# Kernel tuning notes

Measured on AMD Instinct MI355X. Metric: run time of the kernel, lower is better.

The kernel has to match this reference:

```python
import jax, jax.numpy as jnp
import numpy as np

N_NODES = 50000
N_EDGES = 600000
D = 128  # input_nf = output_nf = hidden_nf
EDGE_IN = 2 * D + 1   # source, target, radial
NODE_IN = 2 * D       # x, agg


def _glorot(key, shape):
    fan_in, fan_out = shape[0], shape[1]
    lim = float(np.sqrt(6.0 / (fan_in + fan_out)))
    return jax.random.uniform(key, shape, jnp.float32, -lim, lim)


def setup_inputs() -> dict:
    key = jax.random.key(0)
    ks = jax.random.split(key, 16)
    h = jax.random.normal(ks[0], (N_NODES, D), jnp.float32)
    edge_index = jax.random.randint(ks[1], (2, N_EDGES), 0, N_NODES, jnp.int64 if jax.config.read('jax_enable_x64') else jnp.int32)
    coord = jax.random.uniform(ks[2], (N_NODES, 3), jnp.float32)
    l = jnp.array([10.0, 10.0, 10.0], jnp.float32)  # periodic box lengths (non-trainable buffer)
    return {
        'h': h, 'edge_index': edge_index, 'coord': coord, 'num_nodes': N_NODES, 'l': l,
        # edge_mlp: Linear(257,128) SiLU Linear(128,128) SiLU
        'We1': _glorot(ks[3], (EDGE_IN, D)), 'be1': jnp.zeros((D,), jnp.float32),
        'We2': _glorot(ks[4], (D, D)),       'be2': jnp.zeros((D,), jnp.float32),
        # node_mlp: Linear(256,128) SiLU Linear(128,128)
        'Wn1': _glorot(ks[5], (NODE_IN, D)), 'bn1': jnp.zeros((D,), jnp.float32),
        'Wn2': _glorot(ks[6], (D, D)),       'bn2': jnp.zeros((D,), jnp.float32),
        # coord_mlp: Linear(128,128) SiLU Linear(128,1, bias=False, xavier gain=0.001)
        'Wc1': _glorot(ks[7], (D, D)),       'bc1': jnp.zeros((D,), jnp.float32),
        'Wc2': _glorot(ks[8], (D, 1)) * 0.001,
    }


def reference(h, edge_index, coord, num_nodes, l,
              We1, be1, We2, be2, Wn1, bn1, Wn2, bn2, Wc1, bc1, Wc2):
    row, col = edge_index[0], edge_index[1]

    # coord2radial with periodic minimum-image wrap
    diff = coord[row] - coord[col]                       # [E, 3]
    diff = jnp.where(diff > 0.5 * l, diff - l, diff)
    diff = jnp.where(diff < -0.5 * l, diff + l, diff)
    radial = jnp.sum(diff * diff, axis=1, keepdims=True)  # [E, 1]

    # edge model: gather -> concat -> 2-layer SiLU MLP
    eh = jnp.concatenate([h[row], h[col], radial], axis=1)  # [E, 257]
    eh = jax.nn.silu(eh @ We1 + be1)
    edge_feat = jax.nn.silu(eh @ We2 + be2)                 # [E, 128]

    # coord model: trans/agg computed in the original but discarded (dead code);
    # only the periodic remainder of coord is returned.
    coord_out = jnp.remainder(coord, l)

    # node model: scatter-add edge features into nodes, then MLP + residual
    agg = jax.ops.segment_sum(edge_feat, row, num_segments=num_nodes)  # [N, 128]
    nh = jnp.concatenate([h, agg], axis=1)                              # [N, 256]
    nh = jax.nn.silu(nh @ Wn1 + bn1)
    h_out = h + (nh @ Wn2 + bn2)

    return h_out, coord_out, edge_feat
```

## Files before the change

kernel.cpp:

```cpp
#include <hip/hip_runtime.h>
#include <math.h>

#define D 128
#define SXS 264
#define SHS 132
#define SFS 132

typedef unsigned int u32;
typedef unsigned short u16;
typedef __attribute__((ext_vector_type(8))) short bf16x8;
typedef __attribute__((ext_vector_type(4))) float f32x4;

__device__ __forceinline__ float bfl(u32 u) { return __uint_as_float(u << 16); }
__device__ __forceinline__ float bfh(u32 u) { return __uint_as_float(u & 0xFFFF0000u); }
__device__ __forceinline__ u16 f2bf(float f) {
    u32 u = __float_as_uint(f);
    return (u16)((u + 0x7FFFu + ((u >> 16) & 1u)) >> 16);
}
__device__ __forceinline__ u32 cvt_pk_bf16(float lo, float hi) {
    u32 r;
    asm("v_cvt_pk_bf16_f32 %0, %1, %2" : "=v"(r) : "v"(lo), "v"(hi));
    return r;
}
__device__ __forceinline__ u16 cvt1_bf16(float v) { return (u16)cvt_pk_bf16(v, v); }
__device__ __forceinline__ float silu_f(float x) { return x / (1.0f + __expf(-x)); }

__global__ void coord_kernel(const float* __restrict__ coord,
                             const float* __restrict__ lbox,
                             float* __restrict__ out, int n3) {
    int i = blockIdx.x * 256 + threadIdx.x;
    if (i < n3) {
        float ld = lbox[i % 3];
        float c = coord[i];
        float r = fmodf(c, ld);
        if (r < 0.f) r += ld;
        out[i] = r;
    }
}

__global__ void prep_weights(const float* __restrict__ We1, const float* __restrict__ We2,
                             const float* __restrict__ Wn1, const float* __restrict__ Wn2,
                             u16* __restrict__ wt) {
    int i = blockIdx.x * 256 + threadIdx.x;
    if (i < 32768)        { int n = i >> 8, k = i & 255;              wt[i] = f2bf(We1[(size_t)k*D + n]); }
    else if (i < 49152)   { int j = i - 32768; int n = j >> 7, k = j & 127; wt[i] = f2bf(We2[(size_t)k*D + n]); }
    else if (i < 81920)   { int j = i - 49152; int n = j >> 8, k = j & 255; wt[i] = f2bf(Wn1[(size_t)k*D + n]); }
    else if (i < 98304)   { int j = i - 81920; int n = j >> 7, k = j & 127; wt[i] = f2bf(Wn2[(size_t)k*D + n]); }
}

__global__ void hist_kernel(const int* __restrict__ ei, int* __restrict__ cnt, int E) {
    int e = blockIdx.x * 256 + threadIdx.x;
    if (e < E) atomicAdd(&cnt[ei[e]], 1);
}

__global__ void scan1_kernel(const int* __restrict__ cnt, int* __restrict__ offs,
                             int* __restrict__ bsum, int n ) {
    __shared__ int s[256];
    int t = threadIdx.x, b = blockIdx.x;
    int base = b * 1024 + t * 4;
    int v[4];
    #pragma unroll
    for (int i = 0; i < 4; ++i) { int idx = base + i; v[i] = (idx < n - 1) ? cnt[idx] : 0; }
    int lsum = v[0] + v[1] + v[2] + v[3];
    s[t] = lsum; __syncthreads();
    #pragma unroll
    for (int off = 1; off < 256; off <<= 1) {
        int x = (t >= off) ? s[t - off] : 0; __syncthreads();
        s[t] += x; __syncthreads();
    }
    int run = s[t] - lsum;
    #pragma unroll
    for (int i = 0; i < 4; ++i) { int idx = base + i; if (idx < n) offs[idx] = run; run += v[i]; }
    if (t == 255) bsum[b] = s[255];
}

__global__ void scan2_kernel(int* __restrict__ bsum, int nb) {
    __shared__ int s[64];
    int t = threadIdx.x;
    int orig = (t < nb) ? bsum[t] : 0;
    s[t] = orig; __syncthreads();
    #pragma unroll
    for (int off = 1; off < 64; off <<= 1) {
        int x = (t >= off) ? s[t - off] : 0; __syncthreads();
        s[t] += x; __syncthreads();
    }
    if (t < nb) bsum[t] = s[t] - orig;
}

__global__ void scan3_kernel(int* __restrict__ offs, const int* __restrict__ bsum,
                             int* __restrict__ cursor, int n) {
    int i = blockIdx.x * 256 + threadIdx.x;
    if (i < n) {
        int v = offs[i] + bsum[i >> 10];
        offs[i] = v;
        if (i < n - 1) cursor[i] = v;
    }
}

__global__ void scatter_kernel(const int* __restrict__ ei, int* __restrict__ cursor,
                               int* __restrict__ perm, int4* __restrict__ edata, int E) {
    int e = blockIdx.x * 256 + threadIdx.x;
    if (e < E) {
        int r = ei[e];
        int c = ei[(size_t)E + e];
        int p = atomicAdd(&cursor[r], 1);
        if (edata) edata[p] = make_int4(e, r, c, 0);
        else perm[p] = e;
    }
}

__global__ __launch_bounds__(256, 4) void pq_kernel(
    const float* __restrict__ h, const u16* __restrict__ wt,
    const float* __restrict__ be1,
    u16* __restrict__ Pt, u16* __restrict__ Qt,
    int* __restrict__ cursor, int N)
{
    __shared__ __align__(16) u16 sA[64 * SHS];
    __shared__ __align__(16) u16 sO[64 * SHS];

    const int t = threadIdx.x;
    const int lane = t & 63;
    const int wid = t >> 6;
    const int n0 = blockIdx.x * 64;

    if (t < 64) { int zi = n0 + t; if (zi < N) cursor[zi] = 0; }

    {
        const int e = t & 63, q = t >> 6;
        int ng = n0 + e; int ns = (ng < N) ? ng : N - 1;
        const float4* src = (const float4*)(h + (size_t)ns * D + q * 32);
        u16* dst = sA + e * SHS + q * 32;
        #pragma unroll
        for (int c = 0; c < 4; ++c) {
            float4 a = src[2 * c], b = src[2 * c + 1];
            *(uint4*)(dst + c * 8) = make_uint4(cvt_pk_bf16(a.x, a.y), cvt_pk_bf16(a.z, a.w),
                                               cvt_pk_bf16(b.x, b.y), cvt_pk_bf16(b.z, b.w));
        }
    }
    __syncthreads();

    const int lrow = lane & 15;
    const int kg = lane >> 4;
    const int g4 = kg * 4;
    const int nbase = wid * 32;

    f32x4 accP[4][2] = {}, accQ[4][2] = {};
    {
        bf16x8 Bt[8], Bm[8];
        #pragma unroll
        for (int nn = 0; nn < 2; ++nn)
            #pragma unroll
            for (int s = 0; s < 4; ++s) {
                const u16* bp = wt + (size_t)(nbase + nn * 16 + lrow) * 256 + s * 32 + kg * 8;
                Bt[nn * 4 + s] = *(const bf16x8*)bp;
                Bm[nn * 4 + s] = *(const bf16x8*)(bp + 128);
            }
        #pragma unroll
        for (int s = 0; s < 4; ++s) {
            bf16x8 a[4];
            #pragma unroll
            for (int m = 0; m < 4; ++m)
                a[m] = *(const bf16x8*)(sA + (m * 16 + lrow) * SHS + s * 32 + kg * 8);
            #pragma unroll
            for (int m = 0; m < 4; ++m)
                #pragma unroll
                for (int nn = 0; nn < 2; ++nn) {
                    accP[m][nn] = __builtin_amdgcn_mfma_f32_16x16x32_bf16(a[m], Bt[nn * 4 + s], accP[m][nn], 0, 0, 0);
                    accQ[m][nn] = __builtin_amdgcn_mfma_f32_16x16x32_bf16(a[m], Bm[nn * 4 + s], accQ[m][nn], 0, 0, 0);
                }
        }
    }

    #pragma unroll
    for (int nn = 0; nn < 2; ++nn) {
        int outc = nbase + nn * 16 + lrow;
        float bb = be1[outc];
        #pragma unroll
        for (int m = 0; m < 4; ++m)
            #pragma unroll
            for (int r = 0; r < 4; ++r)
                sO[(m * 16 + g4 + r) * SHS + outc] = cvt1_bf16(accP[m][nn][r] + bb);
    }
    __syncthreads();
    {
        const int f4 = t & 15, rb = t >> 4;
        #pragma unroll
        for (int p = 0; p < 4; ++p) {
            int row = rb + p * 16;
            int ng = n0 + row;
            if (ng < N)
                *(uint4*)(Pt + (size_t)ng * D + f4 * 8) = *(const uint4*)(sO + row * SHS + f4 * 8);
        }
    }
    __syncthreads();
    #pragma unroll
    for (int nn = 0; nn < 2; ++nn) {
        int outc = nbase + nn * 16 + lrow;
        #pragma unroll
        for (int m = 0; m < 4; ++m)
            #pragma unroll
            for (int r = 0; r < 4; ++r)
                sO[(m * 16 + g4 + r) * SHS + outc] = cvt1_bf16(accQ[m][nn][r]);
    }
    __syncthreads();
    {
        const int f4 = t & 15, rb = t >> 4;
        #pragma unroll
        for (int p = 0; p < 4; ++p) {
            int row = rb + p * 16;
            int ng = n0 + row;
            if (ng < N)
                *(uint4*)(Qt + (size_t)ng * D + f4 * 8) = *(const uint4*)(sO + row * SHS + f4 * 8);
        }
    }
}

__global__ __launch_bounds__(256, 8) void edge_pq_kernel(
    const u16* __restrict__ Pt, const u16* __restrict__ Qt,
    const int* __restrict__ ei, const int* __restrict__ perm,
    const int4* __restrict__ edata,
    const float* __restrict__ coord, const float* __restrict__ lbox,
    const u16* __restrict__ wt, const float* __restrict__ We1,
    const float* __restrict__ be2,
    float* __restrict__ ef_out, float* __restrict__ aggf, int E)
{
    __shared__ __align__(16) u16 uni[64 * SHS];
    __shared__ int srow[64], scol[64], sEid[64];
    __shared__ float sRad[64];
    __shared__ float sW[128];
    u16* sH1 = uni;
    u16* sE16 = uni;

    const int t = threadIdx.x;
    const int lane = t & 63;
    const int wid = t >> 6;

    int p0;
    {
        const int nwg = gridDim.x;
        const int orig = blockIdx.x;
        const int q = nwg >> 3, r = nwg & 7;
        const int xcd = orig & 7, idx = orig >> 3;
        const int tile = (xcd < r ? xcd * (q + 1) : r * (q + 1) + (xcd - r) * q) + idx;
        p0 = tile * 64;
    }

    if (t < 64) {
        int slot = p0 + t;
        bool valid = slot < E;
        int cs = valid ? slot : (E - 1);
        int eg, rr, cc;
        if (edata) {
            int4 ed = edata[cs];
            eg = ed.x; rr = ed.y; cc = ed.z;
        } else {
            eg = perm[cs];
            rr = ei[eg];
            cc = ei[(size_t)E + eg];
        }
        sEid[t] = valid ? eg : -1;
        srow[t] = rr;
        scol[t] = cc;
        float rad = 0.f;
        #pragma unroll
        for (int d3 = 0; d3 < 3; ++d3) {
            float df = coord[(size_t)rr * 3 + d3] - coord[(size_t)cc * 3 + d3];
            float ld = lbox[d3];
            df = (df >  0.5f * ld) ? df - ld : df;
            df = (df < -0.5f * ld) ? df + ld : df;
            rad += df * df;
        }
        sRad[t] = rad;
    } else if (t < 192) {
        sW[t - 64] = We1[(size_t)256 * D + (t - 64)];
    }
    __syncthreads();

    {
        const int e = t & 63, q = t >> 6;
        const u16* Pp = Pt + (size_t)srow[e] * D;
        const u16* Qp = Qt + (size_t)scol[e] * D;
        const float rad = sRad[e];
        #pragma unroll
        for (int c0 = 0; c0 < 4; ++c0) {
            int j0 = q * 32 + c0 * 8;
            uint4 pu = *(const uint4*)(Pp + j0);
            uint4 qu = *(const uint4*)(Qp + j0);
            u32 pa[4] = {pu.x, pu.y, pu.z, pu.w};
            u32 qa[4] = {qu.x, qu.y, qu.z, qu.w};
            u32 ow[4];
            #pragma unroll
            for (int k = 0; k < 4; ++k) {
                float w0 = sW[j0 + 2 * k], w1 = sW[j0 + 2 * k + 1];
                float v0 = silu_f(bfl(pa[k]) + bfl(qa[k]) + rad * w0);
                float v1 = silu_f(bfh(pa[k]) + bfh(qa[k]) + rad * w1);
                ow[k] = cvt_pk_bf16(v0, v1);
            }
            *(uint4*)(sH1 + e * SHS + j0) = make_uint4(ow[0], ow[1], ow[2], ow[3]);
        }
    }
    __syncthreads();

    const int lrow = lane & 15;
    const int kg = lane >> 4;
    const int g4 = kg * 4;
    const int nbase = wid * 32;

    f32x4 acc2[4][2] = {};
    {
        bf16x8 B2[8];
        #pragma unroll
        for (int nn = 0; nn < 2; ++nn)
            #pragma unroll
            for (int s = 0; s < 4; ++s)
                B2[nn * 4 + s] = *(const bf16x8*)(wt + 32768 + (size_t)(nbase + nn * 16 + lrow) * 128 + s * 32 + kg * 8);
        #pragma unroll
        for (int s = 0; s < 4; ++s) {
            bf16x8 a[4];
            #pragma unroll
            for (int m = 0; m < 4; ++m)
                a[m] = *(const bf16x8*)(sH1 + (m * 16 + lrow) * SHS + s * 32 + kg * 8);
            #pragma unroll
            for (int m = 0; m < 4; ++m)
                #pragma unroll
                for (int nn = 0; nn < 2; ++nn)
                    acc2[m][nn] = __builtin_amdgcn_mfma_f32_16x16x32_bf16(a[m], B2[nn * 4 + s], acc2[m][nn], 0, 0, 0);
        }
    }
    __syncthreads();

    #pragma unroll
    for (int nn = 0; nn < 2; ++nn) {
        int outc = nbase + nn * 16 + lrow;
        float bb = be2[outc];
        #pragma unroll
        for (int m = 0; m < 4; ++m)
            #pragma unroll
            for (int r = 0; r < 4; ++r)
                sE16[(m * 16 + g4 + r) * SHS + outc] = cvt1_bf16(silu_f(acc2[m][nn][r] + bb));
    }
    __syncthreads();

    {
        const int ct = t & 127;
        const int half = t >> 7;
        const int ebeg = half * 32, eend = ebeg + 32;
        float run = 0.f;
        int prev = srow[ebeg];
        for (int e = ebeg; e < eend; ++e) {
            int r = srow[e];
            if (r != prev) {
                if (run != 0.f) atomicAdd(&aggf[(size_t)prev * D + ct], run);
                run = 0.f; prev = r;
            }
            int eg = sEid[e];
            if (eg >= 0) {
                float v = __uint_as_float((u32)sE16[e * SHS + ct] << 16);
                __builtin_nontemporal_store(v, &ef_out[(size_t)eg * D + ct]);
                run += v;
            }
        }
        if (run != 0.f) atomicAdd(&aggf[(size_t)prev * D + ct], run);
    }
}

__global__ __launch_bounds__(256, 3) void edge_fb_kernel(
    const float* __restrict__ h,
    const int* __restrict__ ei, const int* __restrict__ perm,
    const float* __restrict__ coord, const float* __restrict__ lbox,
    const u16* __restrict__ wt,
    const float* __restrict__ We1, const float* __restrict__ be1,
    const float* __restrict__ be2,
    float* __restrict__ ef_out, float* __restrict__ aggf, int E)
{
    __shared__ __align__(16) u16 sX[64 * SXS];
    __shared__ __align__(16) u16 sH1[64 * SHS];
    __shared__ int srow[64], scol[64], sEid[64];
    __shared__ float sRad[64];

    const int t = threadIdx.x;
    const int lane = t & 63;
    const int wid = t >> 6;

    int p0;
    {
        const int nwg = gridDim.x;
        const int orig = blockIdx.x;
        const int q = nwg >> 3, r = nwg & 7;
        const int xcd = orig & 7, idx = orig >> 3;
        const int tile = (xcd < r ? xcd * (q + 1) : r * (q + 1) + (xcd - r) * q) + idx;
        p0 = tile * 64;
    }

    if (t < 64) {
        int slot = p0 + t;
        int eg = perm[(slot < E) ? slot : (E - 1)];
        sEid[t] = (p0 + t < E) ? eg : -1;
        srow[t] = ei[eg];
        scol[t] = ei[(size_t)E + eg];
    }
    __syncthreads();

    {
        const int e = t & 63;
        const int q = t >> 6;
        const int r = srow[e], c = scol[e];
        const float4* src = (const float4*)((q < 2) ? (h + (size_t)r * D + (q & 1) * 64)
                                                    : (h + (size_t)c * D + (q & 1) * 64));
        u16* dst = sX + e * SXS + q * 64;
        #pragma unroll
        for (int i = 0; i < 8; ++i) {
            float4 a = src[2 * i], b = src[2 * i + 1];
            *(uint4*)(dst + i * 8) = make_uint4(cvt_pk_bf16(a.x, a.y), cvt_pk_bf16(a.z, a.w),
                                               cvt_pk_bf16(b.x, b.y), cvt_pk_bf16(b.z, b.w));
        }
        if (t < 64) {
            int rr = srow[t], cc = scol[t];
            float rad = 0.f;
            #pragma unroll
            for (int d3 = 0; d3 < 3; ++d3) {
                float df = coord[(size_t)rr * 3 + d3] - coord[(size_t)cc * 3 + d3];
                float ld = lbox[d3];
                df = (df >  0.5f * ld) ? df - ld : df;
                df = (df < -0.5f * ld) ? df + ld : df;
                rad += df * df;
            }
            sRad[t] = rad;
        }
    }
    __syncthreads();

    const int lrow = lane & 15;
    const int kg = lane >> 4;
    const int g4 = kg * 4;
    const int nbase = wid * 32;

    f32x4 acc[4][2] = {};
    {
        bf16x8 B1[16];
        #pragma unroll
        for (int nn = 0; nn < 2; ++nn)
            #pragma unroll
            for (int s = 0; s < 8; ++s)
                B1[nn * 8 + s] = *(const bf16x8*)(wt + (size_t)(nbase + nn * 16 + lrow) * 256 + s * 32 + kg * 8);
        #pragma unroll
        for (int s = 0; s < 8; ++s) {
            bf16x8 a[4];
            #pragma unroll
            for (int m = 0; m < 4; ++m)
                a[m] = *(const bf16x8*)(sX + (m * 16 + lrow) * SXS + s * 32 + kg * 8);
            #pragma unroll
            for (int m = 0; m < 4; ++m)
                #pragma unroll
                for (int nn = 0; nn < 2; ++nn)
                    acc[m][nn] = __builtin_amdgcn_mfma_f32_16x16x32_bf16(a[m], B1[nn * 8 + s], acc[m][nn], 0, 0, 0);
        }
    }

    #pragma unroll
    for (int nn = 0; nn < 2; ++nn) {
        int outc = nbase + nn * 16 + lrow;
        float wl = We1[(size_t)256 * D + outc];
        float bb = be1[outc];
        #pragma unroll
        for (int m = 0; m < 4; ++m)
            #pragma unroll
            for (int r = 0; r < 4; ++r) {
                int e = m * 16 + g4 + r;
                float v = acc[m][nn][r] + sRad[e] * wl + bb;
                sH1[e * SHS + outc] = cvt1_bf16(silu_f(v));
            }
    }
    __syncthreads();

    f32x4 acc2[4][2] = {};
    {
        bf16x8 B2[8];
        #pragma unroll
        for (int nn = 0; nn < 2; ++nn)
            #pragma unroll
            for (int s = 0; s < 4; ++s)
                B2[nn * 4 + s] = *(const bf16x8*)(wt + 32768 + (size_t)(nbase + nn * 16 + lrow) * 128 + s * 32 + kg * 8);
        #pragma unroll
        for (int s = 0; s < 4; ++s) {
            bf16x8 a[4];
            #pragma unroll
            for (int m = 0; m < 4; ++m)
                a[m] = *(const bf16x8*)(sH1 + (m * 16 + lrow) * SHS + s * 32 + kg * 8);
            #pragma unroll
            for (int m = 0; m < 4; ++m)
                #pragma unroll
                for (int nn = 0; nn < 2; ++nn)
                    acc2[m][nn] = __builtin_amdgcn_mfma_f32_16x16x32_bf16(a[m], B2[nn * 4 + s], acc2[m][nn], 0, 0, 0);
        }
    }
    __syncthreads();

    float* sXf = (float*)sX;
    #pragma unroll
    for (int nn = 0; nn < 2; ++nn) {
        int outc = nbase + nn * 16 + lrow;
        float bb = be2[outc];
        #pragma unroll
        for (int m = 0; m < 4; ++m)
            #pragma unroll
            for (int r = 0; r < 4; ++r)
                sXf[(m * 16 + g4 + r) * SFS + outc] = silu_f(acc2[m][nn][r] + bb);
    }
    __syncthreads();

    {
        const int ct = t & 127;
        const int half = t >> 7;
        const int ebeg = half * 32, eend = ebeg + 32;
        float run = 0.f;
        int prev = srow[ebeg];
        for (int e = ebeg; e < eend; ++e) {
            int r = srow[e];
            if (r != prev) {
                if (run != 0.f) atomicAdd(&aggf[(size_t)prev * D + ct], run);
                run = 0.f; prev = r;
            }
            int eg = sEid[e];
            if (eg >= 0) {
                float v = sXf[e * SFS + ct];
                __builtin_nontemporal_store(v, &ef_out[(size_t)eg * D + ct]);
                run += v;
            }
        }
        if (run != 0.f) atomicAdd(&aggf[(size_t)prev * D + ct], run);
    }
}

__global__ __launch_bounds__(256, 4) void node_kernel(
    const float* __restrict__ h, const float* __restrict__ aggf,
    const u16* __restrict__ wt,
    const float* __restrict__ bn1, const float* __restrict__ bn2,
    float* __restrict__ h_out, int N)
{
    __shared__ __align__(16) u16 uni[64 * SXS];
    u16* sX = uni;
    u16* sH1 = uni;
    float* sXf = (float*)uni;

    const int t = threadIdx.x;
    const int lane = t & 63;
    const int wid = t >> 6;
    const int n0 = blockIdx.x * 64;

    {
        const int e = t & 63;
        const int q = t >> 6;
        int ng = n0 + e; int ns = (ng < N) ? ng : N - 1;
        const float4* src = (const float4*)(((q < 2) ? h : aggf) + (size_t)ns * D + (q & 1) * 64);
        u16* dst = sX + e * SXS + q * 64;
        #pragma unroll
        for (int i = 0; i < 8; ++i) {
            float4 a = src[2 * i], b = src[2 * i + 1];
            *(uint4*)(dst + i * 8) = make_uint4(cvt_pk_bf16(a.x, a.y), cvt_pk_bf16(a.z, a.w),
                                               cvt_pk_bf16(b.x, b.y), cvt_pk_bf16(b.z, b.w));
        }
    }
    __syncthreads();

    const int lrow = lane & 15;
    const int kg = lane >> 4;
    const int g4 = kg * 4;
    const int nbase = wid * 32;

    f32x4 acc[4][2] = {};
    {
        bf16x8 B1[16];
        #pragma unroll
        for (int nn = 0; nn < 2; ++nn)
            #pragma unroll
            for (int s = 0; s < 8; ++s)
                B1[nn * 8 + s] = *(const bf16x8*)(wt + 49152 + (size_t)(nbase + nn * 16 + lrow) * 256 + s * 32 + kg * 8);
        #pragma unroll
        for (int s = 0; s < 8; ++s) {
            bf16x8 a[4];
            #pragma unroll
            for (int m = 0; m < 4; ++m)
                a[m] = *(const bf16x8*)(sX + (m * 16 + lrow) * SXS + s * 32 + kg * 8);
            #pragma unroll
            for (int m = 0; m < 4; ++m)
                #pragma unroll
                for (int nn = 0; nn < 2; ++nn)
                    acc[m][nn] = __builtin_amdgcn_mfma_f32_16x16x32_bf16(a[m], B1[nn * 8 + s], acc[m][nn], 0, 0, 0);
        }
    }
    __syncthreads();

    #pragma unroll
    for (int nn = 0; nn < 2; ++nn) {
        int outc = nbase + nn * 16 + lrow;
        float bb = bn1[outc];
        #pragma unroll
        for (int m = 0; m < 4; ++m)
            #pragma unroll
            for (int r = 0; r < 4; ++r)
                sH1[(m * 16 + g4 + r) * SHS + outc] = cvt1_bf16(silu_f(acc[m][nn][r] + bb));
    }
    __syncthreads();

    f32x4 acc2[4][2] = {};
    {
        bf16x8 B2[8];
        #pragma unroll
        for (int nn = 0; nn < 2; ++nn)
            #pragma unroll
            for (int s = 0; s < 4; ++s)
                B2[nn * 4 + s] = *(const bf16x8*)(wt + 81920 + (size_t)(nbase + nn * 16 + lrow) * 128 + s * 32 + kg * 8);
        #pragma unroll
        for (int s = 0; s < 4; ++s) {
            bf16x8 a[4];
            #pragma unroll
            for (int m = 0; m < 4; ++m)
                a[m] = *(const bf16x8*)(sH1 + (m * 16 + lrow) * SHS + s * 32 + kg * 8);
            #pragma unroll
            for (int m = 0; m < 4; ++m)
                #pragma unroll
                for (int nn = 0; nn < 2; ++nn)
                    acc2[m][nn] = __builtin_amdgcn_mfma_f32_16x16x32_bf16(a[m], B2[nn * 4 + s], acc2[m][nn], 0, 0, 0);
        }
    }
    __syncthreads();

    #pragma unroll
    for (int nn = 0; nn < 2; ++nn) {
        int outc = nbase + nn * 16 + lrow;
        float bb = bn2[outc];
        #pragma unroll
        for (int m = 0; m < 4; ++m)
            #pragma unroll
            for (int r = 0; r < 4; ++r)
                sXf[(m * 16 + g4 + r) * SFS + outc] = acc2[m][nn][r] + bb;
    }
    __syncthreads();

    {
        const int f4 = t & 31;
        const int nb = t >> 5;
        #pragma unroll
        for (int i = 0; i < 8; ++i) {
            int nl = nb + i * 8;
            int ng = n0 + nl;
            if (ng < N) {
                f32x4 v = *(const f32x4*)&sXf[nl * SFS + f4 * 4];
                const f32x4 hv = *(const f32x4*)&h[(size_t)ng * D + f4 * 4];
                v += hv;
                __builtin_nontemporal_store(v, (f32x4*)&h_out[(size_t)ng * D + f4 * 4]);
            }
        }
    }
}

extern "C" void kernel_launch(void* const* d_in, const int* in_sizes, int n_in,
                              void* d_out, int out_size, void* d_ws, size_t ws_size,
                              hipStream_t stream) {
    const float* h     = (const float*)d_in[0];
    const int*   ei    = (const int*)d_in[1];
    const float* coord = (const float*)d_in[2];
    const float* lbox  = (const float*)d_in[4];
    const float* We1   = (const float*)d_in[5];
    const float* be1   = (const float*)d_in[6];
    const float* We2   = (const float*)d_in[7];
    const float* be2   = (const float*)d_in[8];
    const float* Wn1   = (const float*)d_in[9];
    const float* bn1   = (const float*)d_in[10];
    const float* Wn2   = (const float*)d_in[11];
    const float* bn2   = (const float*)d_in[12];

    const int N = in_sizes[0] / D;
    const int E = in_sizes[1] / 2;

    float* out       = (float*)d_out;
    float* h_out     = out;
    float* coord_out = out + (size_t)N * D;
    float* ef_out    = coord_out + (size_t)N * 3;
    float* aggf      = h_out;

    int* wsi = (int*)d_ws;
    u16* wt     = (u16*)d_ws;
    int* offs   = wsi + 49152;
    int* cursor = offs + (N + 8);
    int* bsum   = cursor + (N + 8);
    int* perm   = bsum + 64;
    u16* Pt     = (u16*)(perm + E);
    u16* Qt     = Pt + (size_t)N * D;
    int4* edata = (int4*)(((uintptr_t)(Qt + (size_t)N * D) + 15) & ~(uintptr_t)15);

    size_t need_pq = (size_t)((char*)(Qt + (size_t)N * D) - (char*)d_ws);
    size_t need_ed = (size_t)((char*)(edata + E) - (char*)d_ws);
    const bool use_pq = ws_size >= need_pq;
    const bool use_ed = use_pq && ws_size >= need_ed;
    int4* edp = use_ed ? edata : nullptr;

    const int nb1 = (N + 1 + 1023) / 1024;

    prep_weights<<<384, 256, 0, stream>>>(We1, We2, Wn1, Wn2, wt);
    if (use_pq)
        pq_kernel<<<(N + 63) / 64, 256, 0, stream>>>(h, wt, be1, Pt, Qt, cursor, N);
    else
        hipMemsetAsync(cursor, 0, (size_t)N * sizeof(int), stream);
    coord_kernel<<<(N * 3 + 255) / 256, 256, 0, stream>>>(coord, lbox, coord_out, N * 3);

    hipMemsetAsync(aggf, 0, (size_t)N * D * sizeof(float), stream);

    hist_kernel<<<(E + 255) / 256, 256, 0, stream>>>(ei, cursor, E);
    scan1_kernel<<<nb1, 256, 0, stream>>>(cursor, offs, bsum, N + 1);
    scan2_kernel<<<1, 64, 0, stream>>>(bsum, nb1);
    scan3_kernel<<<(N + 1 + 255) / 256, 256, 0, stream>>>(offs, bsum, cursor, N + 1);
    scatter_kernel<<<(E + 255) / 256, 256, 0, stream>>>(ei, cursor, perm, edp, E);

    if (use_pq)
        edge_pq_kernel<<<(E + 63) / 64, 256, 0, stream>>>(
            Pt, Qt, ei, perm, edp, coord, lbox, wt, We1, be2, ef_out, aggf, E);
    else
        edge_fb_kernel<<<(E + 63) / 64, 256, 0, stream>>>(
            h, ei, perm, coord, lbox, wt, We1, be1, be2, ef_out, aggf, E);

    node_kernel<<<(N + 63) / 64, 256, 0, stream>>>(
        h, aggf, wt, bn1, bn2, h_out, N);
}
```

Baseline: 271.4 us.

## Accumulate edge aggregation in bf16 via packed atomics and fold coord kernel into pq

Edge-feature aggregation now goes into a bf16 buffer using global_atomic_pk_add_bf16, with each thread handling two channels. This halves the atomic traffic and the memset size, and lets the node kernel load agg already in bf16 without converting it. The coord remainder work is also merged into the pq_kernel launch as extra blocks, removing one launch. The cost is lower accumulation precision: partial sums are rounded to bf16 on every atomic add, which may affect accuracy.

```diff
diff --git a/kernel.cpp b/kernel.cpp
--- a/kernel.cpp
+++ b/kernel.cpp
@@ -10,6 +10,7 @@
 typedef unsigned short u16;
 typedef __attribute__((ext_vector_type(8))) short bf16x8;
 typedef __attribute__((ext_vector_type(4))) float f32x4;
+typedef __attribute__((ext_vector_type(2))) float f32x2;
 
 __device__ __forceinline__ float bfl(u32 u) { return __uint_as_float(u << 16); }
 __device__ __forceinline__ float bfh(u32 u) { return __uint_as_float(u & 0xFFFF0000u); }
@@ -24,6 +25,10 @@
 }
 __device__ __forceinline__ u16 cvt1_bf16(float v) { return (u16)cvt_pk_bf16(v, v); }
 __device__ __forceinline__ float silu_f(float x) { return x / (1.0f + __expf(-x)); }
+__device__ __forceinline__ void atomic_pk_add_bf16(u16* addr, u32 pk) {
+    asm volatile("global_atomic_pk_add_bf16 %0, %1, off sc1"
+                 :: "v"(addr), "v"(pk) : "memory");
+}
 
 __global__ void coord_kernel(const float* __restrict__ coord,
                              const float* __restrict__ lbox,
@@ -113,12 +118,27 @@
     const float* __restrict__ h, const u16* __restrict__ wt,
     const float* __restrict__ be1,
     u16* __restrict__ Pt, u16* __restrict__ Qt,
-    int* __restrict__ cursor, int N)
+    int* __restrict__ cursor, int N,
+    const float* __restrict__ coord, const float* __restrict__ lbox,
+    float* __restrict__ coord_out, int n3, int NBn)
 {
     __shared__ __align__(16) u16 sA[64 * SHS];
     __shared__ __align__(16) u16 sO[64 * SHS];
 
     const int t = threadIdx.x;
+
+    if (blockIdx.x >= NBn) {
+        int i = (blockIdx.x - NBn) * 256 + t;
+        if (i < n3) {
+            float ld = lbox[i % 3];
+            float c = coord[i];
+            float r = fmodf(c, ld);
+            if (r < 0.f) r += ld;
+            coord_out[i] = r;
+        }
+        return;
+    }
+
     const int lane = t & 63;
     const int wid = t >> 6;
     const int n0 = blockIdx.x * 64;
@@ -222,7 +242,8 @@
     const float* __restrict__ coord, const float* __restrict__ lbox,
     const u16* __restrict__ wt, const float* __restrict__ We1,
     const float* __restrict__ be2,
-    float* __restrict__ ef_out, float* __restrict__ aggf, int E)
+    float* __restrict__ ef_out, float* __restrict__ aggf,
+    u16* __restrict__ agg16, int E)
 {
     __shared__ __align__(16) u16 uni[64 * SHS];
     __shared__ int srow[64], scol[64], sEid[64];
@@ -341,7 +362,31 @@
     }
     __syncthreads();
 
-    {
+    if (agg16) {
+        const int cp = t & 63;
+        const int g = t >> 6;
+        const int ebeg = g * 16, eend = ebeg + 16;
+        float r0 = 0.f, r1 = 0.f;
+        int prev = srow[ebeg];
+        for (int e = ebeg; e < eend; ++e) {
+            int r = srow[e];
+            if (r != prev) {
+                if (r0 != 0.f || r1 != 0.f)
+                    atomic_pk_add_bf16(agg16 + (size_t)prev * D + 2 * cp, cvt_pk_bf16(r0, r1));
+                r0 = 0.f; r1 = 0.f; prev = r;
+            }
+            int eg = sEid[e];
+            if (eg >= 0) {
+                u32 pk2 = *(const u32*)(sE16 + e * SHS + 2 * cp);
+                float v0 = bfl(pk2), v1 = bfh(pk2);
+                f32x2 vv = {v0, v1};
+                __builtin_nontemporal_store(vv, (f32x2*)&ef_out[(size_t)eg * D + 2 * cp]);
+                r0 += v0; r1 += v1;
+            }
+        }
+        if (r0 != 0.f || r1 != 0.f)
+            atomic_pk_add_bf16(agg16 + (size_t)prev * D + 2 * cp, cvt_pk_bf16(r0, r1));
+    } else {
         const int ct = t & 127;
         const int half = t >> 7;
         const int ebeg = half * 32, eend = ebeg + 32;
@@ -534,6 +579,7 @@
 
 __global__ __launch_bounds__(256, 4) void node_kernel(
     const float* __restrict__ h, const float* __restrict__ aggf,
+    const u16* __restrict__ agg16,
     const u16* __restrict__ wt,
     const float* __restrict__ bn1, const float* __restrict__ bn2,
     float* __restrict__ h_out, int N)
@@ -552,13 +598,20 @@
         const int e = t & 63;
         const int q = t >> 6;
         int ng = n0 + e; int ns = (ng < N) ? ng : N - 1;
-        const float4* src = (const float4*)(((q < 2) ? h : aggf) + (size_t)ns * D + (q & 1) * 64);
         u16* dst = sX + e * SXS + q * 64;
-        #pragma unroll
-        for (int i = 0; i < 8; ++i) {
-            float4 a = src[2 * i], b = src[2 * i + 1];
-            *(uint4*)(dst + i * 8) = make_uint4(cvt_pk_bf16(a.x, a.y), cvt_pk_bf16(a.z, a.w),
-                                               cvt_pk_bf16(b.x, b.y), cvt_pk_bf16(b.z, b.w));
+        if (q >= 2 && agg16) {
+            const u16* src = agg16 + (size_t)ns * D + (q & 1) * 64;
+            #pragma unroll
+            for (int i = 0; i < 8; ++i)
+                *(uint4*)(dst + i * 8) = *(const uint4*)(src + i * 8);
+        } else {
+            const float4* src = (const float4*)(((q < 2) ? h : aggf) + (size_t)ns * D + (q & 1) * 64);
+            #pragma unroll
+            for (int i = 0; i < 8; ++i) {
+                float4 a = src[2 * i], b = src[2 * i + 1];
+                *(uint4*)(dst + i * 8) = make_uint4(cvt_pk_bf16(a.x, a.y), cvt_pk_bf16(a.z, a.w),
+                                                   cvt_pk_bf16(b.x, b.y), cvt_pk_bf16(b.z, b.w));
+            }
         }
     }
     __syncthreads();
@@ -689,23 +742,34 @@
     u16* Pt     = (u16*)(perm + E);
     u16* Qt     = Pt + (size_t)N * D;
     int4* edata = (int4*)(((uintptr_t)(Qt + (size_t)N * D) + 15) & ~(uintptr_t)15);
-
-    size_t need_pq = (size_t)((char*)(Qt + (size_t)N * D) - (char*)d_ws);
-    size_t need_ed = (size_t)((char*)(edata + E) - (char*)d_ws);
-    const bool use_pq = ws_size >= need_pq;
-    const bool use_ed = use_pq && ws_size >= need_ed;
-    int4* edp = use_ed ? edata : nullptr;
+    u16* agg16  = (u16*)(edata + E);
+
+    size_t need_pq  = (size_t)((char*)(Qt + (size_t)N * D) - (char*)d_ws);
+    size_t need_ed  = (size_t)((char*)(edata + E) - (char*)d_ws);
+    size_t need_a16 = (size_t)((char*)(agg16 + (size_t)N * D) - (char*)d_ws);
+    const bool use_pq  = ws_size >= need_pq;
+    const bool use_ed  = use_pq && ws_size >= need_ed;
+    const bool use_a16 = use_ed && ws_size >= need_a16;
+    int4* edp  = use_ed ? edata : nullptr;
+    u16*  a16p = use_a16 ? agg16 : nullptr;
 
     const int nb1 = (N + 1 + 1023) / 1024;
 
     prep_weights<<<384, 256, 0, stream>>>(We1, We2, Wn1, Wn2, wt);
-    if (use_pq)
-        pq_kernel<<<(N + 63) / 64, 256, 0, stream>>>(h, wt, be1, Pt, Qt, cursor, N);
+    if (use_pq) {
+        const int NBn = (N + 63) / 64;
+        const int NBc = (N * 3 + 255) / 256;
+        pq_kernel<<<NBn + NBc, 256, 0, stream>>>(h, wt, be1, Pt, Qt, cursor, N,
+                                                 coord, lbox, coord_out, N * 3, NBn);
+    } else {
+        hipMemsetAsync(cursor, 0, (size_t)N * sizeof(int), stream);
+        coord_kernel<<<(N * 3 + 255) / 256, 256, 0, stream>>>(coord, lbox, coord_out, N * 3);
+    }
+
+    if (use_a16)
+        hipMemsetAsync(agg16, 0, (size_t)N * D * sizeof(u16), stream);
     else
-        hipMemsetAsync(cursor, 0, (size_t)N * sizeof(int), stream);
-    coord_kernel<<<(N * 3 + 255) / 256, 256, 0, stream>>>(coord, lbox, coord_out, N * 3);
-
-    hipMemsetAsync(aggf, 0, (size_t)N * D * sizeof(float), stream);
+        hipMemsetAsync(aggf, 0, (size_t)N * D * sizeof(float), stream);
 
     hist_kernel<<<(E + 255) / 256, 256, 0, stream>>>(ei, cursor, E);
     scan1_kernel<<<nb1, 256, 0, stream>>>(cursor, offs, bsum, N + 1);
@@ -715,11 +779,11 @@
 
     if (use_pq)
         edge_pq_kernel<<<(E + 63) / 64, 256, 0, stream>>>(
-            Pt, Qt, ei, perm, edp, coord, lbox, wt, We1, be2, ef_out, aggf, E);
+            Pt, Qt, ei, perm, edp, coord, lbox, wt, We1, be2, ef_out, aggf, a16p, E);
     else
         edge_fb_kernel<<<(E + 63) / 64, 256, 0, stream>>>(
             h, ei, perm, coord, lbox, wt, We1, be1, be2, ef_out, aggf, E);
 
     node_kernel<<<(N + 63) / 64, 256, 0, stream>>>(
-        h, aggf, wt, bn1, bn2, h_out, N);
-}
+        h, aggf, a16p, wt, bn1, bn2, h_out, N);
+}
```

Result: faster. 249.7 us (-8.0%).
